# Optimization experiments

Measured on AMD Instinct MI355X. Metric: run time of the kernel, lower is better.

## Reference

```python
import jax, jax.numpy as jnp
import numpy as np

N, E, IN, ED, H, C = 50000, 800000, 128, 32, 4, 32
HC = H * C
SCALE = 1.0 / float(np.sqrt(C))


def _seg_softmax(t, idx, n):
    # t: [E, H], idx: [E] target-node ids -> per-segment softmax over incoming edges
    m = jax.ops.segment_max(t, idx, num_segments=n)
    m = jnp.where(jnp.isfinite(m), m, 0.0)
    e = jnp.exp(t - m[idx])
    z = jax.ops.segment_sum(e, idx, num_segments=n)
    return e / (z[idx] + 1e-16)


def setup_inputs() -> dict:
    key = jax.random.key(0)
    ks = jax.random.split(key, 26)
    w = lambda k, shape: (jax.random.normal(k, shape, jnp.float32) * 0.05)
    return {
        "x": jax.random.normal(ks[0], (N, IN), jnp.float32),
        "edge_index": jax.random.randint(ks[1], (2, E), 0, N),
        "edge_attr": jax.random.normal(ks[2], (E, ED), jnp.float32),
        # DifferentialGraphAttention params (dual QK groups + lambda)
        "Wq1": w(ks[3], (HC, IN)), "Wq2": w(ks[4], (HC, IN)),
        "Wk1": w(ks[5], (HC, IN)), "Wk2": w(ks[6], (HC, IN)),
        "Wvd": w(ks[7], (HC, IN)),
        "Wkr1": w(ks[8], (HC, ED)), "Wkr2": w(ks[9], (HC, ED)),
        "Wvrd": w(ks[10], (HC, ED)),
        "Woutd": w(ks[11], (HC, HC)),
        "lam": jnp.float32(0.8),
        # RelationActivationAttention params
        "Wqa": w(ks[12], (HC, IN)), "Wka": w(ks[13], (HC, IN)), "Wva": w(ks[14], (HC, IN)),
        "Wkra": w(ks[15], (HC, ED)), "Wvra": w(ks[16], (HC, ED)),
        "Wouta": w(ks[17], (HC, HC)),
        # Hybrid fusion params
        "Wproj": w(ks[18], (HC, 2 * HC)), "bproj": jnp.zeros((HC,), jnp.float32),
        "Win": w(ks[19], (HC, IN)), "b_in": jnp.zeros((HC,), jnp.float32),
        "rms_w": jnp.ones((HC,), jnp.float32),
    }


def reference(x, edge_index, edge_attr, Wq1, Wq2, Wk1, Wk2, Wvd, Wkr1, Wkr2, Wvrd,
              Woutd, lam, Wqa, Wka, Wva, Wkra, Wvra, Wouta, Wproj, bproj, Win, b_in,
              rms_w):
    src, dst = edge_index[0], edge_index[1]

    def nproj(W):  # [N, HC] -> [N, H, C]
        return (x @ W.T).reshape(N, H, C)

    def eproj(W):  # [E, HC] -> [E, H, C]
        return (edge_attr @ W.T).reshape(E, H, C)

    # ---- differential relation aggregation branch ----
    Q1, Q2, K1, K2, Vd = nproj(Wq1), nproj(Wq2), nproj(Wk1), nproj(Wk2), nproj(Wvd)
    t1 = jnp.sum(Q1[dst] * (K1[src] + eproj(Wkr1)), axis=-1) * SCALE  # [E, H]
    t2 = jnp.sum(Q2[dst] * (K2[src] + eproj(Wkr2)), axis=-1) * SCALE
    a_diff = _seg_softmax(t1, dst, N) - lam * _seg_softmax(t2, dst, N)
    msg_d = (Vd[src] + eproj(Wvrd)) * a_diff[..., None]               # [E, H, C]
    h_aggr = jax.ops.segment_sum(msg_d, dst, num_segments=N).reshape(N, HC) @ Woutd.T

    # ---- relation activation branch ----
    Qa, Ka, Va = nproj(Wqa), nproj(Wka), nproj(Wva)
    ta = jnp.sum(Qa[dst] * (Ka[src] + eproj(Wkra)), axis=-1) * SCALE  # [E, H]
    a_act = _seg_softmax(ta, dst, N)
    msg_a = (Va[src] + eproj(Wvra)) * a_act[..., None]
    h_actv = jax.ops.segment_sum(msg_a, dst, num_segments=N).reshape(N, HC) @ Wouta.T

    # ---- hybrid fusion + residual + RMSNorm ----
    h = jnp.concatenate([h_aggr, h_actv], axis=-1) @ Wproj.T + bproj
    h = h + (x @ Win.T + b_in)
    h = h * jax.lax.rsqrt(jnp.mean(h * h, axis=-1, keepdims=True) + 1e-6) * rms_w
    return h
```

## Files before the change

kernel.cpp:

```cpp
#include <hip/hip_runtime.h>

typedef unsigned short u16;
typedef unsigned int   u32;
typedef _Float16 half8 __attribute__((ext_vector_type(8)));
typedef _Float16 half2v __attribute__((ext_vector_type(2)));
typedef float    f32x4 __attribute__((ext_vector_type(4)));
typedef unsigned int u32x4 __attribute__((ext_vector_type(4)));
typedef int      i32x2 __attribute__((ext_vector_type(2)));

#define NN 50000
#define EE 800000
#define SCALE 0.17677669529663687f
#define NB 49

#define O_WNODET   0ul
#define O_WFT      393216ul
#define O_WF1      524288ul
#define O_WF3      589824ul
#define O_HIST     655360ul
#define O_BSUM     855360ul
#define O_BOFF     855616ul
#define O_OFF      856064ul
#define O_CUR      1056768ul
#define O_PERM     1257472ul
#define O_NODEQ    7657472ul
#define O_NODEKV   97257472ul
#define O_G        161257472ul

__device__ __forceinline__ float fin(float x){
  return (x == x && fabsf(x) < 3e38f) ? x : 0.f;
}
__device__ __forceinline__ u32 packh(float a, float b){
  union{ u32 u; _Float16 h[2]; } cv; cv.h[0]=(_Float16)a; cv.h[1]=(_Float16)b; return cv.u;
}
union H2U { u32 u; half2v h; };
__device__ __forceinline__ half2v h2(u32 u){ H2U c; c.u=u; return c.h; }

__device__ __forceinline__ u32x4 ntl4(const u32* p){
  return __builtin_nontemporal_load((const u32x4*)p);
}
__device__ __forceinline__ f32x4 ntlf4(const float* p){
  return __builtin_nontemporal_load((const f32x4*)p);
}
__device__ __forceinline__ i32x2 ntl2(const i32x2* p){
  return __builtin_nontemporal_load(p);
}

__global__ __launch_bounds__(256) void prep1(
    const float* __restrict__ Wq1, const float* __restrict__ Wq2, const float* __restrict__ Wqa,
    const float* __restrict__ Wk1, const float* __restrict__ Wk2, const float* __restrict__ Wka,
    const float* __restrict__ Wvd, const float* __restrict__ Wva, const float* __restrict__ Win,
    const float* __restrict__ Wkr1, const float* __restrict__ Wkr2, const float* __restrict__ Wkra,
    const float* __restrict__ Wproj, const float* __restrict__ Woutd, const float* __restrict__ Wouta,
    _Float16* __restrict__ WnodeT, float* __restrict__ Wf1, float* __restrict__ Wf3)
{
  int job = blockIdx.x*256 + threadIdx.x;
  if (job < 1536*128) {
    int n = job >> 7, kk = job & 127;
    int slot = n >> 7, o = n & 127;
    float val;
    if (slot==3 || slot==4 || slot==5) {
      const float* Wkr = (slot==3)?Wkr1:(slot==4)?Wkr2:Wkra;
      const float* Wq  = (slot==3)?Wq1 :(slot==4)?Wq2 :Wqa;
      int h=o>>5, j=o&31;
      float s=0.f;
      for (int c=0;c<32;c++)
        s += Wkr[(h*32+c)*32 + j] * Wq[(h*32+c)*128 + kk];
      val = s;
    } else {
      const float* W = (slot==0)?Wq1:(slot==1)?Wq2:(slot==2)?Wqa:
                       (slot==6)?Wk1:(slot==7)?Wk2:(slot==8)?Wka:
                       (slot==9)?Wvd:(slot==10)?Wva:Win;
      val = W[o*128 + kk];
    }
    WnodeT[n*128 + kk] = (_Float16)fin(val);
  } else {
    int idx = job - 1536*128;
    int which = idx >> 14;
    int r = idx & 16383;
    int o = r >> 7, v = r & 127;
    const float* Wout = which ? Wouta : Woutd;
    float s=0.f;
    for (int u=0;u<128;u++)
      s += Wproj[o*256 + which*128 + u] * Wout[u*128 + v];
    (which?Wf3:Wf1)[o*128+v] = fin(s);
  }
}

__global__ __launch_bounds__(256) void prep2(
    const float* __restrict__ Wf1, const float* __restrict__ Wf3,
    const float* __restrict__ Wvrd, const float* __restrict__ Wvra,
    _Float16* __restrict__ WfT)
{
  int job = blockIdx.x*256 + threadIdx.x;
  int o = job >> 9, kk = job & 511;
  int seg = kk >> 7, v = kk & 127;
  float val;
  if (seg==0) val = Wf1[o*128+v];
  else if (seg==2) val = Wf3[o*128+v];
  else {
    const float* Wf = (seg==1)?Wf1:Wf3;
    const float* Wv = (seg==1)?Wvrd:Wvra;
    int h=v>>5, j=v&31; float s=0.f;
    for (int c=0;c<32;c++)
      s += Wf[o*128 + h*32 + c] * Wv[(h*32+c)*32 + j];
    val = s;
  }
  WfT[o*512 + kk] = (_Float16)fin(val);
}

__global__ __launch_bounds__(256) void gemm_node(
    const float* __restrict__ x, const _Float16* __restrict__ WnodeT,
    const float* __restrict__ b_in,
    _Float16* __restrict__ nodeQ, _Float16* __restrict__ nodeKV)
{
  __shared__ _Float16 As[128][72];
  __shared__ _Float16 Bs[128][72];
  int m0 = blockIdx.x * 128;
  int slot = blockIdx.y;
  int n0 = slot * 128;
  int tid = threadIdx.x;
  int lane = tid & 63, wave = tid >> 6;
  int lm = lane & 15, lq = lane >> 4;
  int mbase = wave*32;
  f32x4 acc[2][8];
  #pragma unroll
  for (int i=0;i<2;i++)
    #pragma unroll
    for (int j=0;j<8;j++) acc[i][j] = (f32x4){0.f,0.f,0.f,0.f};

  for (int kt=0; kt<2; kt++){
    int kk0 = kt*64;
    #pragma unroll
    for (int i=0;i<4;i++){
      int c = tid + i*256;
      int row = c >> 3, kc = (c & 7) * 8;
      int grow = m0 + row;
      half8 hv;
      if (grow < NN){
        float4 v0 = *(const float4*)(x + (size_t)grow*128 + kk0 + kc);
        float4 v1 = *(const float4*)(x + (size_t)grow*128 + kk0 + kc + 4);
        hv[0]=(_Float16)v0.x; hv[1]=(_Float16)v0.y; hv[2]=(_Float16)v0.z; hv[3]=(_Float16)v0.w;
        hv[4]=(_Float16)v1.x; hv[5]=(_Float16)v1.y; hv[6]=(_Float16)v1.z; hv[7]=(_Float16)v1.w;
      } else {
        #pragma unroll
        for (int j=0;j<8;j++) hv[j] = (_Float16)0.f;
      }
      *(half8*)&As[row][kc] = hv;
      *(half8*)&Bs[row][kc] = *(const half8*)(WnodeT + (size_t)(n0+row)*128 + kk0 + kc);
    }
    __syncthreads();
    #pragma unroll
    for (int ks=0; ks<64; ks+=32){
      half8 a0 = *(half8*)&As[mbase + lm][ks + lq*8];
      half8 a1 = *(half8*)&As[mbase + 16 + lm][ks + lq*8];
      #pragma unroll
      for (int ct=0; ct<8; ct++){
        half8 b = *(half8*)&Bs[ct*16 + lm][ks + lq*8];
        acc[0][ct] = __builtin_amdgcn_mfma_f32_16x16x32_f16(a0, b, acc[0][ct], 0,0,0);
        acc[1][ct] = __builtin_amdgcn_mfma_f32_16x16x32_f16(a1, b, acc[1][ct], 0,0,0);
      }
    }
    __syncthreads();
  }
  #pragma unroll
  for (int rt=0; rt<2; rt++){
    #pragma unroll
    for (int reg=0; reg<4; reg++){
      int row = m0 + mbase + rt*16 + lq*4 + reg;
      if (row < NN){
        #pragma unroll
        for (int ct=0; ct<8; ct++){
          int col = ct*16 + lm;
          float bias = (slot == 11) ? b_in[col] : 0.f;
          _Float16 hv = (_Float16)fin(acc[rt][ct][reg] + bias);
          if (slot < 6)
            nodeQ[(size_t)row*896 + slot*128 + col] = hv;
          else if (slot < 11)
            nodeKV[(size_t)row*640 + (slot-6)*128 + col] = hv;
          else
            nodeQ[(size_t)row*896 + 768 + col] = hv;
        }
      }
    }
  }
}

__global__ __launch_bounds__(256) void hist_k(const int* __restrict__ ei, int* __restrict__ hist){
  int e = blockIdx.x*256 + threadIdx.x;
  int d = ei[EE + e];
  if ((unsigned)d < (unsigned)NN) atomicAdd(&hist[d], 1);
}

__global__ __launch_bounds__(1024) void scan1(const int* __restrict__ hist,
                                              int* __restrict__ loc, int* __restrict__ bsum){
  __shared__ int buf[1024];
  int i = blockIdx.x*1024 + threadIdx.x;
  int v = (i < NN) ? hist[i] : 0;
  buf[threadIdx.x] = v;
  __syncthreads();
  int xv = v;
  for (int s = 1; s < 1024; s <<= 1){
    int t = 0;
    if ((int)threadIdx.x >= s) t = buf[threadIdx.x - s];
    __syncthreads();
    xv += t;
    buf[threadIdx.x] = xv;
    __syncthreads();
  }
  if (i < NN) loc[i] = xv - v;
  if (threadIdx.x == 1023) bsum[blockIdx.x] = xv;
}

__global__ __launch_bounds__(64) void scan2(const int* __restrict__ bsum, int* __restrict__ boff){
  int t = threadIdx.x;
  int v = (t < NB) ? bsum[t] : 0;
  int x = v;
  for (int s = 1; s < 64; s <<= 1){
    int u = __shfl_up(x, s);
    if (t >= s) x += u;
  }
  if (t < NB) boff[t] = x - v;
}

__global__ __launch_bounds__(256) void scatter_k(const int* __restrict__ ei,
                                                 const int* __restrict__ loc, const int* __restrict__ boff,
                                                 int* __restrict__ cur, int2* __restrict__ pe2){
  int e = blockIdx.x*256 + threadIdx.x;
  int d = ei[EE + e];
  if ((unsigned)d >= (unsigned)NN) return;
  int pos = loc[d] + boff[d>>10] + atomicAdd(&cur[d], 1);
  if ((unsigned)pos < (unsigned)EE) pe2[pos] = make_int2(e, ei[e]);
}

__global__ __launch_bounds__(64, 4) void attn_k(
    const i32x2* __restrict__ pe2, const int* __restrict__ hist,
    const int* __restrict__ loc, const int* __restrict__ boff,
    const u32* __restrict__ nfQ, const u32* __restrict__ nfKV,
    const float* __restrict__ ea,
    const float* __restrict__ lamp, u32* __restrict__ G, int nbase)
{
  int lane = threadIdx.x & 63;
  int node = nbase + blockIdx.x;
  if (node >= NN) return;
  int E = lane >> 4;
  int l = lane & 15;
  int h = l >> 2;
  const u32* pd = nfQ + (u32)node * 448u;

  int k = hist[node];
  if (k < 0) k = 0;
  if (k > 64) k = 64;
  int o = loc[node] + boff[node>>10];
  if (o < 0) o = 0;

  int pe_e = 0, pe_s = 0;
  if (k > 0){
    int idxl = (lane < k) ? lane : (k-1);
    i32x2 pl = ntl2(&pe2[o + idxl]);
    pe_e = pl[0]; pe_s = pl[1];
  }

  H2U q1[4], q2[4], qa[4], r1[4], r2[4], ra[4];
  {
    u32x4 a = ntl4(pd +        l*4);
    u32x4 b = ntl4(pd +  64 + l*4);
    u32x4 c = ntl4(pd + 128 + l*4);
    q1[0].u=a[0]; q1[1].u=a[1]; q1[2].u=a[2]; q1[3].u=a[3];
    q2[0].u=b[0]; q2[1].u=b[1]; q2[2].u=b[2]; q2[3].u=b[3];
    qa[0].u=c[0]; qa[1].u=c[1]; qa[2].u=c[2]; qa[3].u=c[3];
    int rb = h*16 + (l&3)*4;
    u32x4 d = ntl4(pd + 192 + rb);
    u32x4 e = ntl4(pd + 256 + rb);
    u32x4 f = ntl4(pd + 320 + rb);
    r1[0].u=d[0]; r1[1].u=d[1]; r1[2].u=d[2]; r1[3].u=d[3];
    r2[0].u=e[0]; r2[1].u=e[1]; r2[2].u=e[2]; r2[3].u=e[3];
    ra[0].u=f[0]; ra[1].u=f[1]; ra[2].u=f[2]; ra[3].u=f[3];
  }

  H2U s1v[4], s2v[4], sav[4], s1e[4], s2e[4], sae[4];
  #pragma unroll
  for (int t=0;t<4;t++){ s1v[t].u=0; s2v[t].u=0; sav[t].u=0; s1e[t].u=0; s2e[t].u=0; sae[t].u=0; }
  float z1=0.f, z2=0.f, za=0.f;

  int iters = (k + 3) >> 2;
  for (int it=0; it<iters; it++){
    int eidx = it*4 + E;
    bool valid = eidx < k;
    int sn = __shfl(pe_s, eidx);
    int ee = __shfl(pe_e, eidx);
    if (!valid){ sn = 0; ee = 0; }
    if ((unsigned)sn >= (unsigned)NN) sn = 0;
    if ((unsigned)ee >= (unsigned)EE) ee = 0;
    const u32* ps = nfKV + (u32)sn * 320u + (u32)(l*4);
    u32x4 K1 = *(const u32x4*)(ps);
    u32x4 K2 = *(const u32x4*)(ps + 64);
    u32x4 KA = *(const u32x4*)(ps + 128);
    u32x4 VD = *(const u32x4*)(ps + 192);
    u32x4 VA = *(const u32x4*)(ps + 256);
    f32x4 ef0 = ntlf4(ea + (size_t)ee*32 + (l&3)*8);
    f32x4 ef1 = ntlf4(ea + (size_t)ee*32 + (l&3)*8 + 4);
    half2v e0 = {(_Float16)ef0[0], (_Float16)ef0[1]};
    half2v e1 = {(_Float16)ef0[2], (_Float16)ef0[3]};
    half2v e2 = {(_Float16)ef1[0], (_Float16)ef1[1]};
    half2v e3 = {(_Float16)ef1[2], (_Float16)ef1[3]};

    half2v p1h = q1[0].h*h2(K1[0]) + q1[1].h*h2(K1[1]) + q1[2].h*h2(K1[2]) + q1[3].h*h2(K1[3])
               + r1[0].h*e0 + r1[1].h*e1 + r1[2].h*e2 + r1[3].h*e3;
    half2v p2h = q2[0].h*h2(K2[0]) + q2[1].h*h2(K2[1]) + q2[2].h*h2(K2[2]) + q2[3].h*h2(K2[3])
               + r2[0].h*e0 + r2[1].h*e1 + r2[2].h*e2 + r2[3].h*e3;
    half2v pah = qa[0].h*h2(KA[0]) + qa[1].h*h2(KA[1]) + qa[2].h*h2(KA[2]) + qa[3].h*h2(KA[3])
               + ra[0].h*e0 + ra[1].h*e1 + ra[2].h*e2 + ra[3].h*e3;

    H2U c1, c2, c3, t;
    c1.h = p1h; c2.h = p2h; c3.h = pah;
    t.u = __shfl_xor(c1.u, 1); c1.h += t.h;
    t.u = __shfl_xor(c2.u, 1); c2.h += t.h;
    t.u = __shfl_xor(c3.u, 1); c3.h += t.h;
    t.u = __shfl_xor(c1.u, 2); c1.h += t.h;
    t.u = __shfl_xor(c2.u, 2); c2.h += t.h;
    t.u = __shfl_xor(c3.u, 2); c3.h += t.h;
    float p1 = (float)c1.h[0] + (float)c1.h[1];
    float p2 = (float)c2.h[0] + (float)c2.h[1];
    float pa = (float)c3.h[0] + (float)c3.h[1];

    float w1 = valid ? __expf(p1*SCALE) : 0.f;
    float w2 = valid ? __expf(p2*SCALE) : 0.f;
    float wa = valid ? __expf(pa*SCALE) : 0.f;
    _Float16 w1f = (_Float16)w1, w2f = (_Float16)w2, waf = (_Float16)wa;
    half2v w1h = {w1f, w1f}, w2h = {w2f, w2f}, wah = {waf, waf};

    s1v[0].h += w1h*h2(VD[0]); s1v[1].h += w1h*h2(VD[1]); s1v[2].h += w1h*h2(VD[2]); s1v[3].h += w1h*h2(VD[3]);
    s2v[0].h += w2h*h2(VD[0]); s2v[1].h += w2h*h2(VD[1]); s2v[2].h += w2h*h2(VD[2]); s2v[3].h += w2h*h2(VD[3]);
    sav[0].h += wah*h2(VA[0]); sav[1].h += wah*h2(VA[1]); sav[2].h += wah*h2(VA[2]); sav[3].h += wah*h2(VA[3]);
    s1e[0].h += w1h*e0; s1e[1].h += w1h*e1; s1e[2].h += w1h*e2; s1e[3].h += w1h*e3;
    s2e[0].h += w2h*e0; s2e[1].h += w2h*e1; s2e[2].h += w2h*e2; s2e[3].h += w2h*e3;
    sae[0].h += wah*e0; sae[1].h += wah*e1; sae[2].h += wah*e2; sae[3].h += wah*e3;
    z1 += w1; z2 += w2; za += wa;
  }

  #pragma unroll
  for (int s=16; s<=32; s<<=1){
    H2U t;
    #pragma unroll
    for (int j=0;j<4;j++){
      t.u = __shfl_xor(s1v[j].u, s); s1v[j].h += t.h;
      t.u = __shfl_xor(s2v[j].u, s); s2v[j].h += t.h;
      t.u = __shfl_xor(sav[j].u, s); sav[j].h += t.h;
      t.u = __shfl_xor(s1e[j].u, s); s1e[j].h += t.h;
      t.u = __shfl_xor(s2e[j].u, s); s2e[j].h += t.h;
      t.u = __shfl_xor(sae[j].u, s); sae[j].h += t.h;
    }
    z1 += __shfl_xor(z1, s); z2 += __shfl_xor(z2, s); za += __shfl_xor(za, s);
  }

  if (E == 0){
    float lamv = lamp[0];
    float i1 = 1.f/(z1+1e-16f), i2 = 1.f/(z2+1e-16f), ia = 1.f/(za+1e-16f);
    u32 gb = (u32)node*256u;
    int rb = h*16 + (l&3)*4;
    #pragma unroll
    for (int t=0;t<4;t++){
      float d0 = fin((float)s1v[t].h[0]*i1 - lamv*((float)s2v[t].h[0]*i2));
      float d1 = fin((float)s1v[t].h[1]*i1 - lamv*((float)s2v[t].h[1]*i2));
      G[gb + l*4 + t] = packh(d0, d1);
      float e0v = fin((float)s1e[t].h[0]*i1 - lamv*((float)s2e[t].h[0]*i2));
      float e1v = fin((float)s1e[t].h[1]*i1 - lamv*((float)s2e[t].h[1]*i2));
      G[gb + 64 + rb + t] = packh(e0v, e1v);
      G[gb + 128 + l*4 + t] = packh(fin((float)sav[t].h[0]*ia), fin((float)sav[t].h[1]*ia));
      G[gb + 192 + rb + t] = packh(fin((float)sae[t].h[0]*ia), fin((float)sae[t].h[1]*ia));
    }
  }
}

__global__ __launch_bounds__(256) void gemm_final(
    const _Float16* __restrict__ Gf, const _Float16* __restrict__ WfT,
    const _Float16* __restrict__ nodeQ,
    const float* __restrict__ bproj, const float* __restrict__ rmsw,
    float* __restrict__ out)
{
  __shared__ _Float16 As[64][72];
  __shared__ _Float16 Bs[128][72];
  __shared__ float bS[128], rS[128];
  int m0 = blockIdx.x * 64;
  int tid = threadIdx.x;
  int lane = tid & 63, wave = tid >> 6;
  int lm = lane & 15, lq = lane >> 4;
  int mbase = wave*16;
  if (tid < 128){ bS[tid] = bproj[tid]; rS[tid] = rmsw[tid]; }
  f32x4 acc[8];
  #pragma unroll
  for (int j=0;j<8;j++) acc[j] = (f32x4){0.f,0.f,0.f,0.f};

  for (int kt=0; kt<8; kt++){
    int kk0 = kt*64;
    #pragma unroll
    for (int i=0;i<2;i++){
      int c = tid + i*256;
      int row = c >> 3, kc = (c & 7) * 8;
      int grow = m0 + row;
      half8 av;
      if (grow < NN){
        av = *(const half8*)(Gf + (size_t)grow*512 + kk0 + kc);
      } else {
        #pragma unroll
        for (int j=0;j<8;j++) av[j] = (_Float16)0.f;
      }
      *(half8*)&As[row][kc] = av;
    }
    #pragma unroll
    for (int i=0;i<4;i++){
      int c = tid + i*256;
      int row = c >> 3, kc = (c & 7) * 8;
      *(half8*)&Bs[row][kc] = *(const half8*)(WfT + (size_t)row*512 + kk0 + kc);
    }
    __syncthreads();
    #pragma unroll
    for (int ks=0; ks<64; ks+=32){
      half8 a0 = *(half8*)&As[mbase + lm][ks + lq*8];
      #pragma unroll
      for (int ct=0; ct<8; ct++){
        half8 b = *(half8*)&Bs[ct*16 + lm][ks + lq*8];
        acc[ct] = __builtin_amdgcn_mfma_f32_16x16x32_f16(a0, b, acc[ct], 0,0,0);
      }
    }
    __syncthreads();
  }
  #pragma unroll
  for (int reg=0; reg<4; reg++){
    int row = m0 + mbase + lq*4 + reg;
    bool ok = row < NN;
    float vals[8]; float ss = 0.f;
    #pragma unroll
    for (int ct=0; ct<8; ct++){
      int col = ct*16 + lm;
      float R = ok ? (float)nodeQ[(size_t)row*896 + 768 + col] : 0.f;
      float v = fin(acc[ct][reg] + bS[col] + R);
      vals[ct] = v; ss += v*v;
    }
    #pragma unroll
    for (int sh=1; sh<16; sh<<=1) ss += __shfl_xor(ss, sh);
    float rstd = rsqrtf(ss*(1.0f/128.f) + 1e-6f);
    if (ok){
      #pragma unroll
      for (int ct=0; ct<8; ct++){
        int col = ct*16 + lm;
        out[(size_t)row*128 + col] = fin(vals[ct]*rstd*rS[col]);
      }
    }
  }
}

extern "C" void kernel_launch(void* const* d_in, const int* in_sizes, int n_in,
                              void* d_out, int out_size, void* d_ws, size_t ws_size,
                              hipStream_t stream)
{
  char* w = (char*)d_ws;
  _Float16* WnodeT = (_Float16*)(w + O_WNODET);
  _Float16* WfT    = (_Float16*)(w + O_WFT);
  float*    Wf1    = (float*)(w + O_WF1);
  float*    Wf3    = (float*)(w + O_WF3);
  int*      hist   = (int*)(w + O_HIST);
  int*      bsum   = (int*)(w + O_BSUM);
  int*      boff   = (int*)(w + O_BOFF);
  int*      loc    = (int*)(w + O_OFF);
  int*      cur    = (int*)(w + O_CUR);
  int2*     pe2    = (int2*)(w + O_PERM);
  _Float16* nodeQ  = (_Float16*)(w + O_NODEQ);
  _Float16* nodeKV = (_Float16*)(w + O_NODEKV);
  _Float16* Gf     = (_Float16*)(w + O_G);

  const float* x     = (const float*)d_in[0];
  const int*   ei    = (const int*)d_in[1];
  const float* ea    = (const float*)d_in[2];
  const float* Wq1   = (const float*)d_in[3];
  const float* Wq2   = (const float*)d_in[4];
  const float* Wk1   = (const float*)d_in[5];
  const float* Wk2   = (const float*)d_in[6];
  const float* Wvd   = (const float*)d_in[7];
  const float* Wkr1  = (const float*)d_in[8];
  const float* Wkr2  = (const float*)d_in[9];
  const float* Wvrd  = (const float*)d_in[10];
  const float* Woutd = (const float*)d_in[11];
  const float* lam   = (const float*)d_in[12];
  const float* Wqa   = (const float*)d_in[13];
  const float* Wka   = (const float*)d_in[14];
  const float* Wva   = (const float*)d_in[15];
  const float* Wkra  = (const float*)d_in[16];
  const float* Wvra  = (const float*)d_in[17];
  const float* Wouta = (const float*)d_in[18];
  const float* Wproj = (const float*)d_in[19];
  const float* bproj = (const float*)d_in[20];
  const float* Win   = (const float*)d_in[21];
  const float* b_in  = (const float*)d_in[22];
  const float* rmsw  = (const float*)d_in[23];

  (void)hipMemsetAsync(hist, 0, 50000*sizeof(int), stream);
  (void)hipMemsetAsync(cur,  0, 50000*sizeof(int), stream);

  prep1<<<896, 256, 0, stream>>>(Wq1,Wq2,Wqa, Wk1,Wk2,Wka, Wvd,Wva,Win,
                                 Wkr1,Wkr2,Wkra, Wproj,Woutd,Wouta,
                                 WnodeT, Wf1, Wf3);
  prep2<<<256, 256, 0, stream>>>(Wf1, Wf3, Wvrd, Wvra, WfT);
  gemm_node<<<dim3(391,12), 256, 0, stream>>>(x, WnodeT, b_in, nodeQ, nodeKV);
  hist_k<<<3125, 256, 0, stream>>>(ei, hist);
  scan1<<<NB, 1024, 0, stream>>>(hist, loc, bsum);
  scan2<<<1, 64, 0, stream>>>(bsum, boff);
  scatter_k<<<3125, 256, 0, stream>>>(ei, loc, boff, cur, pe2);
  attn_k<<<12500, 64, 0, stream>>>((const i32x2*)pe2, hist, loc, boff, (const u32*)nodeQ,
                                   (const u32*)nodeKV, ea, lam, (u32*)Gf, 0);
  attn_k<<<12500, 64, 0, stream>>>((const i32x2*)pe2, hist, loc, boff, (const u32*)nodeQ,
                                   (const u32*)nodeKV, ea, lam, (u32*)Gf, 12500);
  attn_k<<<12500, 64, 0, stream>>>((const i32x2*)pe2, hist, loc, boff, (const u32*)nodeQ,
                                   (const u32*)nodeKV, ea, lam, (u32*)Gf, 25000);
  attn_k<<<12500, 64, 0, stream>>>((const i32x2*)pe2, hist, loc, boff, (const u32*)nodeQ,
                                   (const u32*)nodeKV, ea, lam, (u32*)Gf, 37500);
  gemm_final<<<782, 256, 0, stream>>>(Gf, WfT, nodeQ, bproj, rmsw, (float*)d_out);
}
```

Before: 626.8 us.

## Pre-cast x to fp16, stage GEMM epilogue via LDS, merge attention launches

Adds an xcast kernel that converts x to fp16 once, so each of the 12 gemm_node column-slot blocks reads half-size fp16 rows instead of re-reading and re-converting fp32. The gemm_node epilogue now writes accumulators into shared memory and then stores 16-byte vectors, replacing the scattered 2-byte stores. The four attn_k launches are merged into one 50000-block launch to cut launch overhead. xh reuses the G workspace region, which is safe only because G is written later, after gemm_node has finished reading xh.

```diff
diff --git a/kernel.cpp b/kernel.cpp
--- a/kernel.cpp
+++ b/kernel.cpp
@@ -44,6 +44,19 @@
 }
 __device__ __forceinline__ i32x2 ntl2(const i32x2* p){
   return __builtin_nontemporal_load(p);
+}
+
+__global__ __launch_bounds__(256) void xcast(const float* __restrict__ x,
+                                             _Float16* __restrict__ xh)
+{
+  int i = blockIdx.x*256 + threadIdx.x;
+  size_t b = (size_t)i * 8;
+  float4 v0 = *(const float4*)(x + b);
+  float4 v1 = *(const float4*)(x + b + 4);
+  half8 h;
+  h[0]=(_Float16)v0.x; h[1]=(_Float16)v0.y; h[2]=(_Float16)v0.z; h[3]=(_Float16)v0.w;
+  h[4]=(_Float16)v1.x; h[5]=(_Float16)v1.y; h[6]=(_Float16)v1.z; h[7]=(_Float16)v1.w;
+  *(half8*)(xh + b) = h;
 }
 
 __global__ __launch_bounds__(256) void prep1(
@@ -110,12 +123,13 @@
 }
 
 __global__ __launch_bounds__(256) void gemm_node(
-    const float* __restrict__ x, const _Float16* __restrict__ WnodeT,
+    const _Float16* __restrict__ xh, const _Float16* __restrict__ WnodeT,
     const float* __restrict__ b_in,
     _Float16* __restrict__ nodeQ, _Float16* __restrict__ nodeKV)
 {
-  __shared__ _Float16 As[128][72];
-  __shared__ _Float16 Bs[128][72];
+  __shared__ _Float16 S[18432];
+  _Float16 (*As)[72] = (_Float16(*)[72])S;
+  _Float16 (*Bs)[72] = (_Float16(*)[72])(S + 9216);
   int m0 = blockIdx.x * 128;
   int slot = blockIdx.y;
   int n0 = slot * 128;
@@ -138,10 +152,7 @@
       int grow = m0 + row;
       half8 hv;
       if (grow < NN){
-        float4 v0 = *(const float4*)(x + (size_t)grow*128 + kk0 + kc);
-        float4 v1 = *(const float4*)(x + (size_t)grow*128 + kk0 + kc + 4);
-        hv[0]=(_Float16)v0.x; hv[1]=(_Float16)v0.y; hv[2]=(_Float16)v0.z; hv[3]=(_Float16)v0.w;
-        hv[4]=(_Float16)v1.x; hv[5]=(_Float16)v1.y; hv[6]=(_Float16)v1.z; hv[7]=(_Float16)v1.w;
+        hv = *(const half8*)(xh + (size_t)grow*128 + kk0 + kc);
       } else {
         #pragma unroll
         for (int j=0;j<8;j++) hv[j] = (_Float16)0.f;
@@ -163,25 +174,32 @@
     }
     __syncthreads();
   }
+
   #pragma unroll
   for (int rt=0; rt<2; rt++){
     #pragma unroll
     for (int reg=0; reg<4; reg++){
-      int row = m0 + mbase + rt*16 + lq*4 + reg;
-      if (row < NN){
-        #pragma unroll
-        for (int ct=0; ct<8; ct++){
-          int col = ct*16 + lm;
-          float bias = (slot == 11) ? b_in[col] : 0.f;
-          _Float16 hv = (_Float16)fin(acc[rt][ct][reg] + bias);
-          if (slot < 6)
-            nodeQ[(size_t)row*896 + slot*128 + col] = hv;
-          else if (slot < 11)
-            nodeKV[(size_t)row*640 + (slot-6)*128 + col] = hv;
-          else
-            nodeQ[(size_t)row*896 + 768 + col] = hv;
-        }
+      int row = mbase + rt*16 + lq*4 + reg;
+      #pragma unroll
+      for (int ct=0; ct<8; ct++){
+        int col = ct*16 + lm;
+        float bias = (slot == 11) ? b_in[col] : 0.f;
+        S[row*136 + col] = (_Float16)fin(acc[rt][ct][reg] + bias);
       }
+    }
+  }
+  __syncthreads();
+  #pragma unroll
+  for (int i=0;i<8;i++){
+    int idx = tid + i*256;
+    int row = idx >> 4, c8 = (idx & 15)*8;
+    int grow = m0 + row;
+    if (grow < NN){
+      half8 v = *(half8*)&S[row*136 + c8];
+      _Float16* dst = (slot < 6)  ? nodeQ  + (size_t)grow*896 + slot*128 + c8
+                    : (slot < 11) ? nodeKV + (size_t)grow*640 + (slot-6)*128 + c8
+                                  : nodeQ  + (size_t)grow*896 + 768 + c8;
+      *(half8*)dst = v;
     }
   }
 }
@@ -238,10 +256,10 @@
     const int* __restrict__ loc, const int* __restrict__ boff,
     const u32* __restrict__ nfQ, const u32* __restrict__ nfKV,
     const float* __restrict__ ea,
-    const float* __restrict__ lamp, u32* __restrict__ G, int nbase)
+    const float* __restrict__ lamp, u32* __restrict__ G)
 {
   int lane = threadIdx.x & 63;
-  int node = nbase + blockIdx.x;
+  int node = blockIdx.x;
   if (node >= NN) return;
   int E = lane >> 4;
   int l = lane & 15;
@@ -469,6 +487,7 @@
   _Float16* nodeQ  = (_Float16*)(w + O_NODEQ);
   _Float16* nodeKV = (_Float16*)(w + O_NODEKV);
   _Float16* Gf     = (_Float16*)(w + O_G);
+  _Float16* xh     = (_Float16*)(w + O_G);
 
   const float* x     = (const float*)d_in[0];
   const int*   ei    = (const int*)d_in[1];
@@ -498,22 +517,17 @@
   (void)hipMemsetAsync(hist, 0, 50000*sizeof(int), stream);
   (void)hipMemsetAsync(cur,  0, 50000*sizeof(int), stream);
 
+  xcast<<<3125, 256, 0, stream>>>(x, xh);
   prep1<<<896, 256, 0, stream>>>(Wq1,Wq2,Wqa, Wk1,Wk2,Wka, Wvd,Wva,Win,
                                  Wkr1,Wkr2,Wkra, Wproj,Woutd,Wouta,
                                  WnodeT, Wf1, Wf3);
   prep2<<<256, 256, 0, stream>>>(Wf1, Wf3, Wvrd, Wvra, WfT);
-  gemm_node<<<dim3(391,12), 256, 0, stream>>>(x, WnodeT, b_in, nodeQ, nodeKV);
+  gemm_node<<<dim3(391,12), 256, 0, stream>>>(xh, WnodeT, b_in, nodeQ, nodeKV);
   hist_k<<<3125, 256, 0, stream>>>(ei, hist);
   scan1<<<NB, 1024, 0, stream>>>(hist, loc, bsum);
   scan2<<<1, 64, 0, stream>>>(bsum, boff);
   scatter_k<<<3125, 256, 0, stream>>>(ei, loc, boff, cur, pe2);
-  attn_k<<<12500, 64, 0, stream>>>((const i32x2*)pe2, hist, loc, boff, (const u32*)nodeQ,
-                                   (const u32*)nodeKV, ea, lam, (u32*)Gf, 0);
-  attn_k<<<12500, 64, 0, stream>>>((const i32x2*)pe2, hist, loc, boff, (const u32*)nodeQ,
-                                   (const u32*)nodeKV, ea, lam, (u32*)Gf, 12500);
-  attn_k<<<12500, 64, 0, stream>>>((const i32x2*)pe2, hist, loc, boff, (const u32*)nodeQ,
-                                   (const u32*)nodeKV, ea, lam, (u32*)Gf, 25000);
-  attn_k<<<12500, 64, 0, stream>>>((const i32x2*)pe2, hist, loc, boff, (const u32*)nodeQ,
-                                   (const u32*)nodeKV, ea, lam, (u32*)Gf, 37500);
+  attn_k<<<50000, 64, 0, stream>>>((const i32x2*)pe2, hist, loc, boff, (const u32*)nodeQ,
+                                   (const u32*)nodeKV, ea, lam, (u32*)Gf);
   gemm_final<<<782, 256, 0, stream>>>(Gf, WfT, nodeQ, bproj, rmsw, (float*)d_out);
 }
```

Measured after the change: 563.5 us. 10.1% less time.
